# Performance work log

Hardware: AMD Instinct MI355X
Metric: run time of the kernel (lower is better)

Reference implementation:

```python
import jax, jax.numpy as jnp
import numpy as np
from jax import lax

C_EDGE, C_DVS, C_OUT = 128, 128, 128
H, W = 32, 32
MASK_SIZE = 7
THRESH, TAU, GAMA = 1.0, 0.5, 1.0  # LIFSpike defaults (ZIF surrogate)


def _window_mask(h, w, mask_size):
    half = mask_size // 2
    qx = jnp.arange(h)[:, None, None, None]
    qy = jnp.arange(w)[None, :, None, None]
    kx = jnp.arange(h)[None, None, :, None]
    ky = jnp.arange(w)[None, None, None, :]
    allowed = (jnp.abs(kx - qx) <= half) & (jnp.abs(ky - qy) <= half)
    return jnp.where(allowed, 0.0, -10000.0).reshape(h * w, h * w).astype(jnp.float32)


@jax.custom_vjp
def _spike(x):
    return (x > 0).astype(x.dtype)

def _spike_fwd(x):
    return _spike(x), x

def _spike_bwd(x, g):
    # ZIF surrogate: grad = clamp(gama - |x|, 0) / gama^2
    return (g * jnp.clip(GAMA - jnp.abs(x), 0.0, None) / (GAMA * GAMA),)

_spike.defvjp(_spike_fwd, _spike_bwd)


def _lif(x):
    # x: (B, T, C, H, W) -> spikes, scan over time
    xt = jnp.moveaxis(x, 1, 0)  # (T, B, C, H, W)

    def step(mem, inp):
        mem = mem * TAU + inp
        spk = _spike(mem - THRESH)
        mem = (1.0 - spk) * mem
        return mem, spk

    _, spikes = lax.scan(step, jnp.zeros_like(xt[0]), xt)
    return jnp.moveaxis(spikes, 0, 1)


def setup_inputs() -> dict:
    key = jax.random.key(0)
    ks = jax.random.split(key, 16)
    s = 0.05
    return {
        "edge_features": jax.random.normal(ks[0], (8, 4, C_EDGE, H, W), jnp.float32),
        "dvs_features": jax.random.normal(ks[1], (8, 4, C_DVS, H, W), jnp.float32),
        "We": jax.random.normal(ks[2], (C_OUT, C_EDGE), jnp.float32) * s,
        "be": jax.random.normal(ks[3], (C_OUT,), jnp.float32) * s,
        "Wd": jax.random.normal(ks[4], (C_OUT, C_DVS), jnp.float32) * s,
        "bd": jax.random.normal(ks[5], (C_OUT,), jnp.float32) * s,
        "Wq": jax.random.normal(ks[6], (C_OUT, C_OUT), jnp.float32) * s,
        "bq": jax.random.normal(ks[7], (C_OUT,), jnp.float32) * s,
        "Wk": jax.random.normal(ks[8], (C_OUT, C_OUT), jnp.float32) * s,
        "bk": jax.random.normal(ks[9], (C_OUT,), jnp.float32) * s,
        "Wv": jax.random.normal(ks[10], (C_OUT, C_OUT), jnp.float32) * s,
        "bv": jax.random.normal(ks[11], (C_OUT,), jnp.float32) * s,
        "Wf": jax.random.normal(ks[12], (C_OUT, C_OUT), jnp.float32) * s,
        "bf": jax.random.normal(ks[13], (C_OUT,), jnp.float32) * s,
    }


def reference(edge_features, dvs_features, We, be, Wd, bd, Wq, bq, Wk, bk, Wv, bv, Wf, bf):
    B, T, _, h, w = dvs_features.shape
    C = We.shape[0]
    N = h * w
    # 1x1 conv channel alignment (SeqToANNContainer folds B,T)
    ef = (jnp.einsum('btchw,oc->btohw', edge_features, We) + be[None, None, :, None, None]).reshape(B * T, C, h, w)
    df = (jnp.einsum('btchw,oc->btohw', dvs_features, Wd) + bd[None, None, :, None, None]).reshape(B * T, C, h, w)
    # cosine similarity over channels
    l2e = jnp.sqrt(jnp.sum(ef * ef, axis=1, keepdims=True))
    l2d = jnp.sqrt(jnp.sum(df * df, axis=1, keepdims=True))
    sim = jnp.sum((ef / (l2e + 1e-6)) * (df / (l2d + 1e-6)), axis=1, keepdims=True)
    sim = (sim + 1.0) * 0.5
    # density: softmax of edge L2 norm over spatial, scaled by N
    dens = (jax.nn.softmax(l2e.reshape(B * T, N), axis=1) * N).reshape(B * T, 1, h, w)
    ew = (ef * sim).reshape(B * T, C, N)
    dw = (df * dens).reshape(B * T, C, N)
    # conv1d k=1 Q/K/V projections
    q = jnp.einsum('oc,bcn->bon', Wq, ew) + bq[None, :, None]
    k = jnp.einsum('oc,bcn->bon', Wk, dw) + bk[None, :, None]
    v = jnp.einsum('oc,bcn->bon', Wv, dw) + bv[None, :, None]
    mask = _window_mask(h, w, MASK_SIZE)
    attn = jnp.einsum('bcq,bck->bqk', q, k) / (C ** 0.5) + mask[None]
    attn = jax.nn.softmax(attn, axis=-1)
    out = jnp.einsum('bqk,bck->bqc', attn, v)  # (BT, N, C)
    out = out.reshape(B * T, h, w, C).transpose(0, 3, 1, 2).reshape(B, T, C, h, w)
    fused = jnp.einsum('btchw,oc->btohw', out, Wf) + bf[None, None, :, None, None]
    return _lif(fused)
```

## Files before the change

kernel.cpp:

```cpp
#include <hip/hip_runtime.h>
#include <math.h>

#define CC 128
#define NN 1024
#define BTOT 32
#define CP 152
#define PST 232

typedef unsigned short u16;
typedef u16 u16x8 __attribute__((ext_vector_type(8)));
typedef u16 u16x4 __attribute__((ext_vector_type(4)));
typedef __bf16 bf16x8 __attribute__((ext_vector_type(8)));
typedef float f32x4 __attribute__((ext_vector_type(4)));

__device__ __forceinline__ u16 f2b(float f) {
    unsigned int u = __float_as_uint(f);
    u += 0x7FFFu + ((u >> 16) & 1u);
    return (u16)(u >> 16);
}
__device__ __forceinline__ float b2f(u16 u) {
    return __uint_as_float(((unsigned int)u) << 16);
}

__device__ __forceinline__ void loadB(const u16* brow, int g, bf16x8 bfr[4]) {
#pragma unroll
    for (int kk = 0; kk < 4; ++kk)
        bfr[kk] = *(const bf16x8*)(brow + kk * 32 + g * 8);
}
__device__ __forceinline__ bf16x8 ldA(const u16* __restrict__ WB, int ot, int kk, int l) {
    return *(const bf16x8*)(WB + ((size_t)(ot * 4 + kk) * 64 + l) * 8);
}

__global__ __launch_bounds__(128) void k_comp(
    const float* __restrict__ Wq, const float* __restrict__ Wk,
    const float* __restrict__ Wv, const float* __restrict__ We,
    const float* __restrict__ Wd, const float* __restrict__ be,
    const float* __restrict__ bd,
    float* __restrict__ Wcomp, float* __restrict__ cvec)
{
    const int mat = blockIdx.y, o = blockIdx.x, c = threadIdx.x;
    const float* A = (mat == 0) ? Wq : (mat == 1) ? Wk : Wv;
    const float* B = (mat == 0) ? We : Wd;
    const float* bv = (mat == 0) ? be : bd;
    float acc = 0.f;
    for (int m = 0; m < CC; ++m) acc += A[o * CC + m] * B[m * CC + c];
    Wcomp[(size_t)mat * 16384 + o * CC + c] = acc;
    if (c == 0) {
        float bacc = 0.f;
        for (int m = 0; m < CC; ++m) bacc += A[o * CC + m] * bv[m];
        cvec[mat * CC + o] = bacc;
    }
}

__global__ __launch_bounds__(256) void k_wcvt(
    const float* __restrict__ W0, const float* __restrict__ W1,
    const float* __restrict__ W2, const float* __restrict__ W3,
    const float* __restrict__ W4, const float* __restrict__ W5,
    u16* __restrict__ out)
{
    const int gid = blockIdx.x * 256 + threadIdx.x;
    const int wi = gid >> 11, rem = gid & 2047;
    const float* W = (wi == 0) ? W0 : (wi == 1) ? W1 : (wi == 2) ? W2
                   : (wi == 3) ? W3 : (wi == 4) ? W4 : W5;
    const int ot = rem >> 8, kk = (rem >> 6) & 3, l = rem & 63;
    const int row = ot * 16 + (l & 15), col = kk * 32 + (l >> 4) * 8;
    float4 a = *(const float4*)(W + row * CC + col);
    float4 b = *(const float4*)(W + row * CC + col + 4);
    u16x8 u;
    u[0] = f2b(a.x); u[1] = f2b(a.y); u[2] = f2b(a.z); u[3] = f2b(a.w);
    u[4] = f2b(b.x); u[5] = f2b(b.y); u[6] = f2b(b.z); u[7] = f2b(b.w);
    *(u16x8*)(out + (size_t)wi * 16384 + ((size_t)(ot * 4 + kk) * 64 + l) * 8) = u;
}

__global__ __launch_bounds__(256) void k_front(
    const float* __restrict__ edge, const float* __restrict__ dvs,
    const u16* __restrict__ WeB, const u16* __restrict__ WdB,
    const u16* __restrict__ WqeB, const u16* __restrict__ WkdB,
    const u16* __restrict__ WvdB,
    const float* __restrict__ be, const float* __restrict__ bd,
    const float* __restrict__ bq,
    const float* __restrict__ cq, const float* __restrict__ ck,
    const float* __restrict__ cv,
    float* __restrict__ l2e_out,
    u16* __restrict__ qT, u16* __restrict__ kT, u16* __restrict__ vN)
{
    __shared__ u16 bufA[64 * CP];
    __shared__ u16 bufB[64 * CP];
    const int t = threadIdx.x;
    const int bt = blockIdx.y;
    const int n0b = blockIdx.x * 64;
    const float* eb = edge + (size_t)bt * CC * NN + n0b;
    const float* db = dvs + (size_t)bt * CC * NN + n0b;

#pragma unroll
    for (int j = 0; j < 2; ++j) {
        const int i = t + 256 * j;
        const int c4 = i >> 4, p = i & 15;
        float4 e[4], d[4];
#pragma unroll
        for (int m = 0; m < 4; ++m) {
            e[m] = *(const float4*)(eb + (size_t)(4 * c4 + m) * NN + 4 * p);
            d[m] = *(const float4*)(db + (size_t)(4 * c4 + m) * NN + 4 * p);
        }
#pragma unroll
        for (int n = 0; n < 4; ++n) {
            u16x4 ue, ud;
            ue[0] = f2b(((const float*)&e[0])[n]); ud[0] = f2b(((const float*)&d[0])[n]);
            ue[1] = f2b(((const float*)&e[1])[n]); ud[1] = f2b(((const float*)&d[1])[n]);
            ue[2] = f2b(((const float*)&e[2])[n]); ud[2] = f2b(((const float*)&d[2])[n]);
            ue[3] = f2b(((const float*)&e[3])[n]); ud[3] = f2b(((const float*)&d[3])[n]);
            *(u16x4*)&bufA[(4 * p + n) * CP + 4 * c4] = ue;
            *(u16x4*)&bufB[(4 * p + n) * CP + 4 * c4] = ud;
        }
    }
    __syncthreads();

    const int l = t & 63, w = t >> 6;
    const int l15 = l & 15, g = l >> 4;
    const int nloc = w * 16 + l15;
    const size_t gn = (size_t)bt * NN + n0b + nloc;

    bf16x8 bfrE[4], bfrD[4];
    loadB(bufA + nloc * CP, g, bfrE);
    loadB(bufB + nloc * CP, g, bfrD);

    f32x4 aE[8], aD[8];
#pragma unroll
    for (int ot = 0; ot < 8; ++ot) {
        aE[ot] = *(const f32x4*)(be + 16 * ot + 4 * g);
        aD[ot] = *(const f32x4*)(bd + 16 * ot + 4 * g);
    }
#pragma unroll
    for (int ot = 0; ot < 8; ++ot)
#pragma unroll
        for (int kk = 0; kk < 4; ++kk) {
            aE[ot] = __builtin_amdgcn_mfma_f32_16x16x32_bf16(ldA(WeB, ot, kk, l), bfrE[kk], aE[ot], 0, 0, 0);
            aD[ot] = __builtin_amdgcn_mfma_f32_16x16x32_bf16(ldA(WdB, ot, kk, l), bfrD[kk], aD[ot], 0, 0, 0);
        }
    float s2e = 0.f, s2d = 0.f, sed = 0.f;
#pragma unroll
    for (int ot = 0; ot < 8; ++ot)
#pragma unroll
        for (int r = 0; r < 4; ++r) {
            const float fe = aE[ot][r], fd = aD[ot][r];
            s2e += fe * fe; s2d += fd * fd; sed += fe * fd;
        }
    s2e += __shfl_xor(s2e, 16); s2e += __shfl_xor(s2e, 32);
    s2d += __shfl_xor(s2d, 16); s2d += __shfl_xor(s2d, 32);
    sed += __shfl_xor(sed, 16); sed += __shfl_xor(sed, 32);
    const float le = sqrtf(s2e), ld = sqrtf(s2d);
    const float sim = (sed / ((le + 1e-6f) * (ld + 1e-6f)) + 1.0f) * 0.5f;
    if (g == 0) l2e_out[gn] = le;

    {
        f32x4 aQ[8];
#pragma unroll
        for (int ot = 0; ot < 8; ++ot) aQ[ot] = *(const f32x4*)(cq + 16 * ot + 4 * g);
#pragma unroll
        for (int ot = 0; ot < 8; ++ot)
#pragma unroll
            for (int kk = 0; kk < 4; ++kk)
                aQ[ot] = __builtin_amdgcn_mfma_f32_16x16x32_bf16(ldA(WqeB, ot, kk, l), bfrE[kk], aQ[ot], 0, 0, 0);
#pragma unroll
        for (int ot = 0; ot < 8; ++ot) {
            f32x4 b4 = *(const f32x4*)(bq + 16 * ot + 4 * g);
            u16x4 u;
#pragma unroll
            for (int r = 0; r < 4; ++r) u[r] = f2b(sim * aQ[ot][r] + b4[r]);
            *(u16x4*)(qT + gn * CC + 16 * ot + 4 * g) = u;
        }
    }
    {
        f32x4 aK[8];
#pragma unroll
        for (int ot = 0; ot < 8; ++ot) aK[ot] = *(const f32x4*)(ck + 16 * ot + 4 * g);
#pragma unroll
        for (int ot = 0; ot < 8; ++ot)
#pragma unroll
            for (int kk = 0; kk < 4; ++kk)
                aK[ot] = __builtin_amdgcn_mfma_f32_16x16x32_bf16(ldA(WkdB, ot, kk, l), bfrD[kk], aK[ot], 0, 0, 0);
#pragma unroll
        for (int ot = 0; ot < 8; ++ot) {
            u16x4 u;
#pragma unroll
            for (int r = 0; r < 4; ++r) u[r] = f2b(aK[ot][r]);
            *(u16x4*)(kT + gn * CC + 16 * ot + 4 * g) = u;
        }
    }
    {
        f32x4 aV[8];
#pragma unroll
        for (int ot = 0; ot < 8; ++ot) aV[ot] = *(const f32x4*)(cv + 16 * ot + 4 * g);
#pragma unroll
        for (int ot = 0; ot < 8; ++ot)
#pragma unroll
            for (int kk = 0; kk < 4; ++kk)
                aV[ot] = __builtin_amdgcn_mfma_f32_16x16x32_bf16(ldA(WvdB, ot, kk, l), bfrD[kk], aV[ot], 0, 0, 0);
#pragma unroll
        for (int ot = 0; ot < 8; ++ot)
#pragma unroll
            for (int r = 0; r < 4; ++r)
                vN[((size_t)bt * CC + 16 * ot + 4 * g + r) * NN + n0b + nloc] = f2b(aV[ot][r]);
    }
}

__global__ __launch_bounds__(256) void k_dens(const float* __restrict__ l2e,
                                              float* __restrict__ dens)
{
    __shared__ float red1[4];
    __shared__ float red2[4];
    const int bt = blockIdx.x, t = threadIdx.x;
    const int lane = t & 63, wid = t >> 6;
    const float* x = l2e + (size_t)bt * NN;
    float v[4], m = -1e30f;
#pragma unroll
    for (int i = 0; i < 4; ++i) { v[i] = x[t + 256 * i]; m = fmaxf(m, v[i]); }
#pragma unroll
    for (int off = 32; off >= 1; off >>= 1) m = fmaxf(m, __shfl_xor(m, off));
    if (lane == 0) red1[wid] = m;
    __syncthreads();
    m = fmaxf(fmaxf(red1[0], red1[1]), fmaxf(red1[2], red1[3]));
    float e[4], s = 0.f;
#pragma unroll
    for (int i = 0; i < 4; ++i) { e[i] = expf(v[i] - m); s += e[i]; }
#pragma unroll
    for (int off = 32; off >= 1; off >>= 1) s += __shfl_xor(s, off);
    if (lane == 0) red2[wid] = s;
    __syncthreads();
    s = red2[0] + red2[1] + red2[2] + red2[3];
    const float scale = 1024.0f / s;
#pragma unroll
    for (int i = 0; i < 4; ++i) dens[(size_t)bt * NN + t + 256 * i] = e[i] * scale;
}

__global__ __launch_bounds__(256) void k_attn(
    const u16* __restrict__ qT, const u16* __restrict__ kT,
    const u16* __restrict__ vN, const float* __restrict__ dens,
    const float* __restrict__ bk, const float* __restrict__ bv,
    u16* __restrict__ attT)
{
    __shared__ u16 P_all[4 * 32 * PST];
    const int t = threadIdx.x;
    const int id = blockIdx.x;
    const int bt = (id & 7) * 4 + (id >> 6);
    const int qx = ((id >> 3) & 7) * 4 + (t >> 6);
    const int l = t & 63, l15 = l & 15, g = l >> 4;
    u16* P = P_all + (t >> 6) * 32 * PST;
    const size_t btNN = (size_t)bt * NN;
    const float invsq = 0.08838834764831843f;

    u16x8 ql[2][4];
#pragma unroll
    for (int nt = 0; nt < 2; ++nt)
#pragma unroll
        for (int kk = 0; kk < 4; ++kk)
            ql[nt][kk] = *(const u16x8*)(qT + (btNN + qx * 32 + 16 * nt + l15) * CC + 32 * kk + 8 * g);

    float qbk[2] = {0.f, 0.f};
#pragma unroll
    for (int kk = 0; kk < 4; ++kk) {
        f32x4 b0 = *(const f32x4*)(bk + 32 * kk + 8 * g);
        f32x4 b1 = *(const f32x4*)(bk + 32 * kk + 8 * g + 4);
#pragma unroll
        for (int nt = 0; nt < 2; ++nt)
#pragma unroll
            for (int j = 0; j < 4; ++j) {
                qbk[nt] += b2f(ql[nt][kk][j]) * b0[j];
                qbk[nt] += b2f(ql[nt][kk][4 + j]) * b1[j];
            }
    }
#pragma unroll
    for (int nt = 0; nt < 2; ++nt) {
        qbk[nt] += __shfl_xor(qbk[nt], 16);
        qbk[nt] += __shfl_xor(qbk[nt], 32);
    }

    float ssum[2] = {0.f, 0.f};
#pragma unroll
    for (int i = 0; i < 7; ++i) {
        const int kxr = qx - 3 + i;
        const int kxc = min(max(kxr, 0), 31);
        const bool cval = (kxr == kxc);
        f32x4 acc[2][2];
#pragma unroll
        for (int mt = 0; mt < 2; ++mt)
#pragma unroll
            for (int nt = 0; nt < 2; ++nt) acc[mt][nt] = (f32x4){0.f, 0.f, 0.f, 0.f};
#pragma unroll
        for (int kk = 0; kk < 4; ++kk)
#pragma unroll
            for (int mt = 0; mt < 2; ++mt) {
                bf16x8 ka = *(const bf16x8*)(kT + (btNN + kxc * 32 + 16 * mt + l15) * CC + 32 * kk + 8 * g);
#pragma unroll
                for (int nt = 0; nt < 2; ++nt)
                    acc[mt][nt] = __builtin_amdgcn_mfma_f32_16x16x32_bf16(
                        ka, __builtin_bit_cast(bf16x8, ql[nt][kk]), acc[mt][nt], 0, 0, 0);
            }
#pragma unroll
        for (int mt = 0; mt < 2; ++mt) {
            f32x4 d4 = *(const f32x4*)(dens + btNN + kxc * 32 + 16 * mt + 4 * g);
#pragma unroll
            for (int nt = 0; nt < 2; ++nt) {
                const int qyv = l15 + 16 * nt;
                u16x4 pw;
#pragma unroll
                for (int r = 0; r < 4; ++r) {
                    const float s = (d4[r] * acc[mt][nt][r] + qbk[nt]) * invsq;
                    const int ky = 16 * mt + 4 * g + r;
                    const int dy = ky - qyv;
                    const bool vld = cval && (dy >= -3) && (dy <= 3);
                    const float e = vld ? __expf(s) : 0.f;
                    ssum[nt] += e;
                    pw[r] = f2b(e * d4[r]);
                }
                *(u16x4*)&P[qyv * PST + i * 32 + 16 * mt + 4 * g] = pw;
            }
        }
    }
    float inv[2];
#pragma unroll
    for (int nt = 0; nt < 2; ++nt) {
        float s = ssum[nt];
        s += __shfl_xor(s, 16);
        s += __shfl_xor(s, 32);
        inv[nt] = 1.0f / s;
    }
    asm volatile("s_waitcnt lgkmcnt(0)" ::: "memory");
    __builtin_amdgcn_sched_barrier(0);

    f32x4 o[8][2];
#pragma unroll
    for (int mt = 0; mt < 8; ++mt)
#pragma unroll
        for (int nt = 0; nt < 2; ++nt) o[mt][nt] = (f32x4){0.f, 0.f, 0.f, 0.f};
#pragma unroll
    for (int i = 0; i < 7; ++i) {
        const int kxc = min(max(qx - 3 + i, 0), 31);
        bf16x8 pb[2];
#pragma unroll
        for (int nt = 0; nt < 2; ++nt)
            pb[nt] = *(const bf16x8*)&P[(16 * nt + l15) * PST + i * 32 + 8 * g];
#pragma unroll
        for (int mt = 0; mt < 8; ++mt) {
            bf16x8 va = *(const bf16x8*)(vN + ((size_t)bt * CC + 16 * mt + l15) * NN + kxc * 32 + 8 * g);
#pragma unroll
            for (int nt = 0; nt < 2; ++nt)
                o[mt][nt] = __builtin_amdgcn_mfma_f32_16x16x32_bf16(va, pb[nt], o[mt][nt], 0, 0, 0);
        }
    }
#pragma unroll
    for (int mt = 0; mt < 8; ++mt) {
        f32x4 bv4 = *(const f32x4*)(bv + 16 * mt + 4 * g);
#pragma unroll
        for (int nt = 0; nt < 2; ++nt) {
            u16x4 ov;
#pragma unroll
            for (int r = 0; r < 4; ++r) ov[r] = f2b(o[mt][nt][r] * inv[nt] + bv4[r]);
            *(u16x4*)(attT + (btNN + qx * 32 + 16 * nt + l15) * CC + 16 * mt + 4 * g) = ov;
        }
    }
}

__global__ __launch_bounds__(128) void k_flif(
    const u16* __restrict__ attT, const u16* __restrict__ WfB,
    const float* __restrict__ bf, float* __restrict__ out)
{
    __shared__ float spk[128 * 36];
    const int t = threadIdx.x;
    const int n0b = blockIdx.x * 32;
    const int b = blockIdx.y;
    const int l = t & 63, w = t >> 6;
    const int l15 = l & 15, g = l >> 4;
    const int nloc = w * 16 + l15;
    f32x4 mem[8];
#pragma unroll
    for (int ot = 0; ot < 8; ++ot) mem[ot] = (f32x4){0.f, 0.f, 0.f, 0.f};

    for (int tt = 0; tt < 4; ++tt) {
        const u16* brow = attT + ((size_t)(b * 4 + tt) * NN + n0b + nloc) * CC;
        bf16x8 bfr[4];
#pragma unroll
        for (int kk = 0; kk < 4; ++kk)
            bfr[kk] = *(const bf16x8*)(brow + kk * 32 + g * 8);
#pragma unroll
        for (int ot = 0; ot < 8; ++ot) {
            f32x4 a = *(const f32x4*)(bf + 16 * ot + 4 * g);
#pragma unroll
            for (int kk = 0; kk < 4; ++kk)
                a = __builtin_amdgcn_mfma_f32_16x16x32_bf16(
                    *(const bf16x8*)(WfB + ((size_t)(ot * 4 + kk) * 64 + l) * 8),
                    bfr[kk], a, 0, 0, 0);
            f32x4 mv = mem[ot] * 0.5f + a;
#pragma unroll
            for (int r = 0; r < 4; ++r) {
                const float s = (mv[r] > 1.0f) ? 1.0f : 0.0f;
                spk[(16 * ot + 4 * g + r) * 36 + nloc] = s;
                if (mv[r] > 1.0f) mv[r] = 0.f;
            }
            mem[ot] = mv;
        }
        __syncthreads();
#pragma unroll
        for (int j = 0; j < 8; ++j) {
            const int i = t + 128 * j;
            const int row = i >> 3, n4 = (i & 7) * 4;
            *(float4*)(out + ((size_t)(b * 4 + tt) * CC + row) * NN + n0b + n4) =
                *(const float4*)&spk[row * 36 + n4];
        }
        __syncthreads();
    }
}

extern "C" void kernel_launch(void* const* d_in, const int* in_sizes, int n_in,
                              void* d_out, int out_size, void* d_ws, size_t ws_size,
                              hipStream_t stream) {
    (void)in_sizes; (void)n_in; (void)out_size; (void)ws_size;
    const float* edge = (const float*)d_in[0];
    const float* dvs  = (const float*)d_in[1];
    const float* We = (const float*)d_in[2];
    const float* be = (const float*)d_in[3];
    const float* Wd = (const float*)d_in[4];
    const float* bd = (const float*)d_in[5];
    const float* Wq = (const float*)d_in[6];
    const float* bq = (const float*)d_in[7];
    const float* Wk = (const float*)d_in[8];
    const float* bk = (const float*)d_in[9];
    const float* Wv = (const float*)d_in[10];
    const float* bv = (const float*)d_in[11];
    const float* Wf = (const float*)d_in[12];
    const float* bf = (const float*)d_in[13];
    float* out = (float*)d_out;

    const size_t S = (size_t)BTOT * NN * CC;
    u16* qT   = (u16*)d_ws;
    u16* kT   = qT + S;
    u16* vN   = kT + S;
    u16* attT = vN + S;
    u16* WbAll = attT + S;
    float* fbase = (float*)(WbAll + 6 * 16384);
    float* Wcomp = fbase;
    float* cvec  = Wcomp + 3 * 16384;
    float* l2e   = cvec + 3 * CC;
    float* dens  = l2e + BTOT * NN;
    u16* WeB  = WbAll + 0 * 16384;
    u16* WdB  = WbAll + 1 * 16384;
    u16* WqeB = WbAll + 2 * 16384;
    u16* WkdB = WbAll + 3 * 16384;
    u16* WvdB = WbAll + 4 * 16384;
    u16* WfB  = WbAll + 5 * 16384;
    float* cq = cvec;
    float* ck = cvec + CC;
    float* cv = cvec + 2 * CC;

    k_comp<<<dim3(128, 3), 128, 0, stream>>>(Wq, Wk, Wv, We, Wd, be, bd, Wcomp, cvec);
    k_wcvt<<<48, 256, 0, stream>>>(We, Wd, Wcomp, Wcomp + 16384, Wcomp + 32768, Wf, WbAll);
    k_front<<<dim3(16, BTOT), 256, 0, stream>>>(edge, dvs, WeB, WdB, WqeB, WkdB, WvdB,
                                                be, bd, bq, cq, ck, cv, l2e, qT, kT, vN);
    k_dens<<<BTOT, 256, 0, stream>>>(l2e, dens);
    k_attn<<<256, 256, 0, stream>>>(qT, kT, vN, dens, bk, bv, attT);
    k_flif<<<dim3(32, 8), 128, 0, stream>>>(attT, WfB, bf, out);
}
```

Before: 71.42 us.

## Fuse attention with output projection and LIF, remap blocks to time steps

```diff
diff --git a/kernel.cpp b/kernel.cpp
--- a/kernel.cpp
+++ b/kernel.cpp
@@ -5,7 +5,9 @@
 #define NN 1024
 #define BTOT 32
 #define CP 152
-#define PST 232
+#define PSTs 40
+#define CPA 136
+#define CQS 36
 
 typedef unsigned short u16;
 typedef u16 u16x8 __attribute__((ext_vector_type(8)));
@@ -196,11 +198,21 @@
 #pragma unroll
             for (int kk = 0; kk < 4; ++kk)
                 aV[ot] = __builtin_amdgcn_mfma_f32_16x16x32_bf16(ldA(WvdB, ot, kk, l), bfrD[kk], aV[ot], 0, 0, 0);
+        __syncthreads();
+        u16* bufT = bufA;
 #pragma unroll
         for (int ot = 0; ot < 8; ++ot)
 #pragma unroll
             for (int r = 0; r < 4; ++r)
-                vN[((size_t)bt * CC + 16 * ot + 4 * g + r) * NN + n0b + nloc] = f2b(aV[ot][r]);
+                bufT[(16 * ot + 4 * g + r) * 72 + nloc] = f2b(aV[ot][r]);
+        __syncthreads();
+#pragma unroll
+        for (int p = 0; p < 4; ++p) {
+            const int idx = t + 256 * p;
+            const int c = idx >> 3, n8 = (idx & 7) * 8;
+            *(u16x8*)(vN + ((size_t)bt * CC + c) * NN + n0b + n8) =
+                *(const u16x8*)&bufT[c * 72 + n8];
+        }
     }
 }
 
@@ -233,19 +245,23 @@
     for (int i = 0; i < 4; ++i) dens[(size_t)bt * NN + t + 256 * i] = e[i] * scale;
 }
 
-__global__ __launch_bounds__(256) void k_attn(
+__global__ __launch_bounds__(256) void k_attnf(
     const u16* __restrict__ qT, const u16* __restrict__ kT,
     const u16* __restrict__ vN, const float* __restrict__ dens,
     const float* __restrict__ bk, const float* __restrict__ bv,
-    u16* __restrict__ attT)
+    const u16* __restrict__ WfB, const float* __restrict__ bf,
+    float* __restrict__ out)
 {
-    __shared__ u16 P_all[4 * 32 * PST];
+    __shared__ u16 lds_u16[26624];
     const int t = threadIdx.x;
     const int id = blockIdx.x;
-    const int bt = (id & 7) * 4 + (id >> 6);
-    const int qx = ((id >> 3) & 7) * 4 + (t >> 6);
+    const int b = id & 7, qx = id >> 3;
+    const int w = t >> 6;
+    const int bt = b * 4 + w;
     const int l = t & 63, l15 = l & 15, g = l >> 4;
-    u16* P = P_all + (t >> 6) * 32 * PST;
+    u16* att = lds_u16;
+    float* convq = (float*)(lds_u16 + 17408);
+    u16* P = lds_u16 + w * 32 * PSTs;
     const size_t btNN = (size_t)bt * NN;
     const float invsq = 0.08838834764831843f;
 
@@ -276,6 +292,12 @@
     }
 
     float ssum[2] = {0.f, 0.f};
+    f32x4 o[8][2];
+#pragma unroll
+    for (int mt = 0; mt < 8; ++mt)
+#pragma unroll
+        for (int nt = 0; nt < 2; ++nt) o[mt][nt] = (f32x4){0.f, 0.f, 0.f, 0.f};
+
 #pragma unroll
     for (int i = 0; i < 7; ++i) {
         const int kxr = qx - 3 + i;
@@ -313,8 +335,21 @@
                     ssum[nt] += e;
                     pw[r] = f2b(e * d4[r]);
                 }
-                *(u16x4*)&P[qyv * PST + i * 32 + 16 * mt + 4 * g] = pw;
+                *(u16x4*)&P[qyv * PSTs + 16 * mt + 4 * g] = pw;
             }
+        }
+        asm volatile("s_waitcnt lgkmcnt(0)" ::: "memory");
+        __builtin_amdgcn_sched_barrier(0);
+        bf16x8 pb[2];
+#pragma unroll
+        for (int nt = 0; nt < 2; ++nt)
+            pb[nt] = *(const bf16x8*)&P[(16 * nt + l15) * PSTs + 8 * g];
+#pragma unroll
+        for (int mt = 0; mt < 8; ++mt) {
+            bf16x8 va = *(const bf16x8*)(vN + ((size_t)bt * CC + 16 * mt + l15) * NN + kxc * 32 + 8 * g);
+#pragma unroll
+            for (int nt = 0; nt < 2; ++nt)
+                o[mt][nt] = __builtin_amdgcn_mfma_f32_16x16x32_bf16(va, pb[nt], o[mt][nt], 0, 0, 0);
         }
     }
     float inv[2];
@@ -325,87 +360,66 @@
         s += __shfl_xor(s, 32);
         inv[nt] = 1.0f / s;
     }
+
+    __syncthreads();
+
+    u16* attw = att + w * 32 * CPA;
+#pragma unroll
+    for (int mt = 0; mt < 8; ++mt) {
+        f32x4 bv4 = *(const f32x4*)(bv + 16 * mt + 4 * g);
+#pragma unroll
+        for (int nt = 0; nt < 2; ++nt) {
+            u16x4 ov;
+#pragma unroll
+            for (int r = 0; r < 4; ++r) ov[r] = f2b(o[mt][nt][r] * inv[nt] + bv4[r]);
+            *(u16x4*)&attw[(16 * nt + l15) * CPA + 16 * mt + 4 * g] = ov;
+        }
+    }
     asm volatile("s_waitcnt lgkmcnt(0)" ::: "memory");
     __builtin_amdgcn_sched_barrier(0);
 
-    f32x4 o[8][2];
-#pragma unroll
-    for (int mt = 0; mt < 8; ++mt)
-#pragma unroll
-        for (int nt = 0; nt < 2; ++nt) o[mt][nt] = (f32x4){0.f, 0.f, 0.f, 0.f};
-#pragma unroll
-    for (int i = 0; i < 7; ++i) {
-        const int kxc = min(max(qx - 3 + i, 0), 31);
-        bf16x8 pb[2];
+    bf16x8 cb[4][2];
+#pragma unroll
+    for (int kk = 0; kk < 4; ++kk)
 #pragma unroll
         for (int nt = 0; nt < 2; ++nt)
-            pb[nt] = *(const bf16x8*)&P[(16 * nt + l15) * PST + i * 32 + 8 * g];
-#pragma unroll
-        for (int mt = 0; mt < 8; ++mt) {
-            bf16x8 va = *(const bf16x8*)(vN + ((size_t)bt * CC + 16 * mt + l15) * NN + kxc * 32 + 8 * g);
+            cb[kk][nt] = *(const bf16x8*)&attw[(16 * nt + l15) * CPA + 32 * kk + 8 * g];
+
+    const int cl = t >> 3, n4 = (t & 7) * 4;
+#pragma unroll
+    for (int cr = 0; cr < 4; ++cr) {
+#pragma unroll
+        for (int oi = 0; oi < 2; ++oi) {
+            const int ot = 2 * cr + oi;
+            f32x4 ca[2];
+#pragma unroll
+            for (int nt = 0; nt < 2; ++nt) ca[nt] = *(const f32x4*)(bf + 16 * ot + 4 * g);
+#pragma unroll
+            for (int kk = 0; kk < 4; ++kk) {
+                bf16x8 afr = ldA(WfB, ot, kk, l);
+#pragma unroll
+                for (int nt = 0; nt < 2; ++nt)
+                    ca[nt] = __builtin_amdgcn_mfma_f32_16x16x32_bf16(afr, cb[kk][nt], ca[nt], 0, 0, 0);
+            }
 #pragma unroll
             for (int nt = 0; nt < 2; ++nt)
-                o[mt][nt] = __builtin_amdgcn_mfma_f32_16x16x32_bf16(va, pb[nt], o[mt][nt], 0, 0, 0);
-        }
-    }
-#pragma unroll
-    for (int mt = 0; mt < 8; ++mt) {
-        f32x4 bv4 = *(const f32x4*)(bv + 16 * mt + 4 * g);
-#pragma unroll
-        for (int nt = 0; nt < 2; ++nt) {
-            u16x4 ov;
-#pragma unroll
-            for (int r = 0; r < 4; ++r) ov[r] = f2b(o[mt][nt][r] * inv[nt] + bv4[r]);
-            *(u16x4*)(attT + (btNN + qx * 32 + 16 * nt + l15) * CC + 16 * mt + 4 * g) = ov;
-        }
-    }
-}
-
-__global__ __launch_bounds__(128) void k_flif(
-    const u16* __restrict__ attT, const u16* __restrict__ WfB,
-    const float* __restrict__ bf, float* __restrict__ out)
-{
-    __shared__ float spk[128 * 36];
-    const int t = threadIdx.x;
-    const int n0b = blockIdx.x * 32;
-    const int b = blockIdx.y;
-    const int l = t & 63, w = t >> 6;
-    const int l15 = l & 15, g = l >> 4;
-    const int nloc = w * 16 + l15;
-    f32x4 mem[8];
-#pragma unroll
-    for (int ot = 0; ot < 8; ++ot) mem[ot] = (f32x4){0.f, 0.f, 0.f, 0.f};
-
-    for (int tt = 0; tt < 4; ++tt) {
-        const u16* brow = attT + ((size_t)(b * 4 + tt) * NN + n0b + nloc) * CC;
-        bf16x8 bfr[4];
-#pragma unroll
-        for (int kk = 0; kk < 4; ++kk)
-            bfr[kk] = *(const bf16x8*)(brow + kk * 32 + g * 8);
-#pragma unroll
-        for (int ot = 0; ot < 8; ++ot) {
-            f32x4 a = *(const f32x4*)(bf + 16 * ot + 4 * g);
-#pragma unroll
-            for (int kk = 0; kk < 4; ++kk)
-                a = __builtin_amdgcn_mfma_f32_16x16x32_bf16(
-                    *(const bf16x8*)(WfB + ((size_t)(ot * 4 + kk) * 64 + l) * 8),
-                    bfr[kk], a, 0, 0, 0);
-            f32x4 mv = mem[ot] * 0.5f + a;
-#pragma unroll
-            for (int r = 0; r < 4; ++r) {
-                const float s = (mv[r] > 1.0f) ? 1.0f : 0.0f;
-                spk[(16 * ot + 4 * g + r) * 36 + nloc] = s;
-                if (mv[r] > 1.0f) mv[r] = 0.f;
-            }
-            mem[ot] = mv;
+#pragma unroll
+                for (int r = 0; r < 4; ++r)
+                    convq[w * 32 * CQS + (16 * oi + 4 * g + r) * CQS + 16 * nt + l15] = ca[nt][r];
         }
         __syncthreads();
-#pragma unroll
-        for (int j = 0; j < 8; ++j) {
-            const int i = t + 128 * j;
-            const int row = i >> 3, n4 = (i & 7) * 4;
-            *(float4*)(out + ((size_t)(b * 4 + tt) * CC + row) * NN + n0b + n4) =
-                *(const float4*)&spk[row * 36 + n4];
+        f32x4 mem = {0.f, 0.f, 0.f, 0.f};
+#pragma unroll
+        for (int tt = 0; tt < 4; ++tt) {
+            f32x4 x = *(const f32x4*)&convq[tt * 32 * CQS + cl * CQS + n4];
+            f32x4 mv = mem * 0.5f + x;
+            float4 sp;
+            sp.x = (mv[0] > 1.0f) ? 1.0f : 0.0f; if (mv[0] > 1.0f) mv[0] = 0.f;
+            sp.y = (mv[1] > 1.0f) ? 1.0f : 0.0f; if (mv[1] > 1.0f) mv[1] = 0.f;
+            sp.z = (mv[2] > 1.0f) ? 1.0f : 0.0f; if (mv[2] > 1.0f) mv[2] = 0.f;
+            sp.w = (mv[3] > 1.0f) ? 1.0f : 0.0f; if (mv[3] > 1.0f) mv[3] = 0.f;
+            *(float4*)(out + ((size_t)(b * 4 + tt) * CC + 32 * cr + cl) * NN + qx * 32 + n4) = sp;
+            mem = mv;
         }
         __syncthreads();
     }
@@ -435,8 +449,7 @@
     u16* qT   = (u16*)d_ws;
     u16* kT   = qT + S;
     u16* vN   = kT + S;
-    u16* attT = vN + S;
-    u16* WbAll = attT + S;
+    u16* WbAll = vN + S;
     float* fbase = (float*)(WbAll + 6 * 16384);
     float* Wcomp = fbase;
     float* cvec  = Wcomp + 3 * 16384;
@@ -457,6 +470,5 @@
     k_front<<<dim3(16, BTOT), 256, 0, stream>>>(edge, dvs, WeB, WdB, WqeB, WkdB, WvdB,
                                                 be, bd, bq, cq, ck, cv, l2e, qT, kT, vN);
     k_dens<<<BTOT, 256, 0, stream>>>(l2e, dens);
-    k_attn<<<256, 256, 0, stream>>>(qT, kT, vN, dens, bk, bv, attT);
-    k_flif<<<dim3(32, 8), 128, 0, stream>>>(attT, WfB, bf, out);
-}
+    k_attnf<<<256, 256, 0, stream>>>(qT, kT, vN, dens, bk, bv, WfB, bf, out);
+}
```

After: 68.95 us. 1.04x faster.
